# Kernel optimization log

Hardware: AMD Instinct MI355X
Metric: run time of the kernel (lower is better)

The kernel has to match this reference:

```python
import jax, jax.numpy as jnp
import numpy as np

SIGMA_MAX = 25.0

def marginal_prob_std(t):
    # VE-SDE std: sqrt((sigma_max^(2t) - 1) / (2 ln sigma_max))
    log_s = jnp.log(SIGMA_MAX)
    return jnp.sqrt((jnp.exp(2.0 * t * log_s) - 1.0) / (2.0 * log_s))

def setup_inputs() -> dict:
    key = jax.random.key(0)
    k1, k2, k3 = jax.random.split(key, 3)
    B, N, d = 16384, 16384, 1
    x = jax.random.normal(k1, (B, d), dtype=jnp.float32)
    t = jax.random.uniform(k2, (B,), dtype=jnp.float32, minval=1e-3, maxval=1.0)
    train_data = jax.random.normal(k3, (N, d), dtype=jnp.float32)
    return {"x": x, "t": t, "train_data": train_data}

def reference(x, t, train_data):
    # x: [B,1], t: [B], train_data: [N,1]
    sigma = marginal_prob_std(t)                       # [B]
    sigma2 = sigma * sigma                             # [B]
    # pairwise squared distance (d=1): [N, B]
    diff = train_data - x[:, 0][None, :]               # [N,1]-[1,B] -> broadcast fails; do explicit
    diff = train_data[:, 0][:, None] - x[:, 0][None, :]  # [N, B]
    pdf = jnp.exp(-0.5 * (diff * diff) / sigma2[None, :])  # [N, B]
    num = jnp.sum(pdf * train_data, axis=0)            # [N,B]*[N,1] -> [B]
    den = jnp.sum(pdf, axis=0)                         # [B]
    den_safe = jnp.where(den == 0.0, 1.0, den)
    evals = jnp.where(den == 0.0, 0.0, num / den_safe) # nan -> 0 as in torch code
    evals = evals[:, None]                             # [B,1]
    return (evals - x) / sigma2[:, None]
```

## Files before the change

### kernel.cpp

```cpp
#include <hip/hip_runtime.h>
#include <math.h>


typedef float v2f __attribute__((ext_vector_type(2)));
typedef float v8f __attribute__((ext_vector_type(8)));

#define BLK 256
#define CH  256
#define JPB (2 * BLK)

#if __has_builtin(__builtin_amdgcn_exp2f)
#define EXP2(x) __builtin_amdgcn_exp2f(x)
#else
#define EXP2(x) exp2f(x)
#endif

__device__ __forceinline__ float sigma2_of(float tj) {
  const float TWO_LOG_S = 6.4377516497364011f;
  return (__expf(TWO_LOG_S * tj) - 1.0f) / TWO_LOG_S;
}

template <bool ATOMIC>
__launch_bounds__(BLK)
__global__ void gmm_partial(const float* __restrict__ x,
                            const float* __restrict__ t,
                            const float* __restrict__ td,
                            float* __restrict__ ws,
                            int N, int B) {
  const int tid  = threadIdx.x;
  const int j0   = blockIdx.x * JPB + tid;
  const int j1   = j0 + BLK;
  const int s    = blockIdx.y;
  const int S    = gridDim.y;
  const int base = s * CH;
  const float* __restrict__ tp = td + base;
  const int lim = (N - base < CH) ? (N - base) : CH;

  const float HALF_LOG2E = 0.72134752044448170f;
  float r0 = 0.f, y0 = 0.f, r1 = 0.f, y1 = 0.f;
  if (j0 < B) { r0 = __fsqrt_rn(HALF_LOG2E / sigma2_of(t[j0])); y0 = x[j0] * r0; }
  if (j1 < B) { r1 = __fsqrt_rn(HALF_LOG2E / sigma2_of(t[j1])); y1 = x[j1] * r1; }

  const v2f rv0 = {r0, r0}, ny0 = {-y0, -y0};
  const v2f rv1 = {r1, r1}, ny1 = {-y1, -y1};

  v2f nA0 = {0,0}, nB0 = {0,0}, dA0 = {0,0}, dB0 = {0,0};
  v2f nA1 = {0,0}, nB1 = {0,0}, dA1 = {0,0}, dB1 = {0,0};

  auto body = [&](v2f g, const v2f& rv, const v2f& ny, v2f& nacc, v2f& dacc) {
    v2f d = __builtin_elementwise_fma(g, rv, ny);
    v2f q = d * d;
    v2f p;
    p.x = EXP2(-q.x);
    p.y = EXP2(-q.y);
    dacc += p;
    nacc = __builtin_elementwise_fma(p, g, nacc);
  };

  if (lim == CH) {
    #pragma unroll 2
    for (int i = 0; i < CH; i += 8) {
      v8f f = *(const v8f*)(tp + i);
      v2f g0 = {f[0], f[1]}, g1 = {f[2], f[3]};
      v2f g2 = {f[4], f[5]}, g3 = {f[6], f[7]};
      body(g0, rv0, ny0, nA0, dA0);
      body(g1, rv0, ny0, nB0, dB0);
      body(g2, rv0, ny0, nA0, dA0);
      body(g3, rv0, ny0, nB0, dB0);
      body(g0, rv1, ny1, nA1, dA1);
      body(g1, rv1, ny1, nB1, dB1);
      body(g2, rv1, ny1, nA1, dA1);
      body(g3, rv1, ny1, nB1, dB1);
    }
  } else {
    for (int i = 0; i < CH; i += 8) {
      v8f f;
      #pragma unroll
      for (int k = 0; k < 8; ++k) f[k] = (i + k < lim) ? tp[i + k] : 1e30f;
      v2f g0 = {f[0], f[1]}, g1 = {f[2], f[3]};
      v2f g2 = {f[4], f[5]}, g3 = {f[6], f[7]};
      body(g0, rv0, ny0, nA0, dA0);
      body(g1, rv0, ny0, nB0, dB0);
      body(g2, rv0, ny0, nA0, dA0);
      body(g3, rv0, ny0, nB0, dB0);
      body(g0, rv1, ny1, nA1, dA1);
      body(g1, rv1, ny1, nB1, dB1);
      body(g2, rv1, ny1, nA1, dA1);
      body(g3, rv1, ny1, nB1, dB1);
    }
  }

  v2f nv0 = nA0 + nB0, dv0 = dA0 + dB0;
  v2f nv1 = nA1 + nB1, dv1 = dA1 + dB1;
  float num0 = nv0.x + nv0.y, den0 = dv0.x + dv0.y;
  float num1 = nv1.x + nv1.y, den1 = dv1.x + dv1.y;

  if (ATOMIC) {
    if (j0 < B) { atomicAdd(&ws[j0], num0); atomicAdd(&ws[B + j0], den0); }
    if (j1 < B) { atomicAdd(&ws[j1], num1); atomicAdd(&ws[B + j1], den1); }
  } else {
    if (j0 < B) {
      ws[(size_t)s * B + j0]       = num0;
      ws[(size_t)(S + s) * B + j0] = den0;
    }
    if (j1 < B) {
      ws[(size_t)s * B + j1]       = num1;
      ws[(size_t)(S + s) * B + j1] = den1;
    }
  }
}

__global__ void gmm_final(const float* __restrict__ x,
                          const float* __restrict__ t,
                          const float* __restrict__ ws,
                          float* __restrict__ out, int B, int S) {
  int j = blockIdx.x * blockDim.x + threadIdx.x;
  if (j >= B) return;
  float num = 0.f, den = 0.f;
  for (int s = 0; s < S; ++s) {
    num += ws[(size_t)s * B + j];
    den += ws[(size_t)(S + s) * B + j];
  }
  float sigma2 = sigma2_of(t[j]);
  float evals = (den == 0.0f) ? 0.0f : (num / den);
  out[j] = (evals - x[j]) / sigma2;
}

__global__ void zero_kernel(float* __restrict__ p, int n) {
  int i = blockIdx.x * blockDim.x + threadIdx.x;
  if (i < n) p[i] = 0.0f;
}

extern "C" void kernel_launch(void* const* d_in, const int* in_sizes, int n_in,
                              void* d_out, int out_size, void* d_ws, size_t ws_size,
                              hipStream_t stream) {
  const float* x  = (const float*)d_in[0];
  const float* t  = (const float*)d_in[1];
  const float* td = (const float*)d_in[2];
  float* out = (float*)d_out;
  float* ws  = (float*)d_ws;

  const int B = in_sizes[0];
  const int N = in_sizes[2];

  const int S = (N + CH - 1) / CH;
  size_t need = (size_t)2 * S * B * sizeof(float);

  if (ws_size >= need) {
    dim3 grid((B + JPB - 1) / JPB, S);
    gmm_partial<false><<<grid, BLK, 0, stream>>>(x, t, td, ws, N, B);
    gmm_final<<<(B + BLK - 1) / BLK, BLK, 0, stream>>>(x, t, ws, out, B, S);
  } else {
    int nzero = 2 * B;
    zero_kernel<<<(nzero + 255) / 256, 256, 0, stream>>>(ws, nzero);
    dim3 grid((B + JPB - 1) / JPB, S);
    gmm_partial<true><<<grid, BLK, 0, stream>>>(x, t, td, ws, N, B);
    gmm_final<<<(B + BLK - 1) / BLK, BLK, 0, stream>>>(x, t, ws, out, B, 1);
  }
}
```

Measured before the change: 109.7 us.

## Process four outputs per thread with halved data chunks and software prefetch

Each thread now handles four B columns instead of two, so every loaded train_data value is reused across more outputs. The chunk size per block row is halved, giving twice as many partial slices, and the full-chunk loop prefetches the next 8-float vector before processing the current one. The aim is better amortization of loads and more independent exp work per thread. In exchange the partial workspace and the final reduction grow, and register pressure rises.

```diff
diff --git a/kernel.cpp b/kernel.cpp
--- a/kernel.cpp
+++ b/kernel.cpp
@@ -6,8 +6,9 @@
 typedef float v8f __attribute__((ext_vector_type(8)));
 
 #define BLK 256
-#define CH  256
-#define JPB (2 * BLK)
+#define CH  128
+#define JPT 4
+#define JPB (JPT * BLK)
 
 #if __has_builtin(__builtin_amdgcn_exp2f)
 #define EXP2(x) __builtin_amdgcn_exp2f(x)
@@ -28,84 +29,84 @@
                             float* __restrict__ ws,
                             int N, int B) {
   const int tid  = threadIdx.x;
-  const int j0   = blockIdx.x * JPB + tid;
-  const int j1   = j0 + BLK;
   const int s    = blockIdx.y;
   const int S    = gridDim.y;
   const int base = s * CH;
   const float* __restrict__ tp = td + base;
-  const int lim = (N - base < CH) ? (N - base) : CH;
 
   const float HALF_LOG2E = 0.72134752044448170f;
-  float r0 = 0.f, y0 = 0.f, r1 = 0.f, y1 = 0.f;
-  if (j0 < B) { r0 = __fsqrt_rn(HALF_LOG2E / sigma2_of(t[j0])); y0 = x[j0] * r0; }
-  if (j1 < B) { r1 = __fsqrt_rn(HALF_LOG2E / sigma2_of(t[j1])); y1 = x[j1] * r1; }
+  int   j[JPT];
+  v2f   rv[JPT], ny[JPT];
+  #pragma unroll
+  for (int k = 0; k < JPT; ++k) {
+    j[k] = blockIdx.x * JPB + k * BLK + tid;
+    float r = 0.f, y = 0.f;
+    if (j[k] < B) {
+      r = __fsqrt_rn(HALF_LOG2E / sigma2_of(t[j[k]]));
+      y = x[j[k]] * r;
+    }
+    rv[k].x = r;  rv[k].y = r;
+    ny[k].x = -y; ny[k].y = -y;
+  }
 
-  const v2f rv0 = {r0, r0}, ny0 = {-y0, -y0};
-  const v2f rv1 = {r1, r1}, ny1 = {-y1, -y1};
+  v2f nacc[JPT][2], dacc[JPT][2];
+  #pragma unroll
+  for (int k = 0; k < JPT; ++k)
+    #pragma unroll
+    for (int c = 0; c < 2; ++c) {
+      nacc[k][c].x = 0.f; nacc[k][c].y = 0.f;
+      dacc[k][c].x = 0.f; dacc[k][c].y = 0.f;
+    }
 
-  v2f nA0 = {0,0}, nB0 = {0,0}, dA0 = {0,0}, dB0 = {0,0};
-  v2f nA1 = {0,0}, nB1 = {0,0}, dA1 = {0,0}, dB1 = {0,0};
-
-  auto body = [&](v2f g, const v2f& rv, const v2f& ny, v2f& nacc, v2f& dacc) {
-    v2f d = __builtin_elementwise_fma(g, rv, ny);
-    v2f q = d * d;
-    v2f p;
-    p.x = EXP2(-q.x);
-    p.y = EXP2(-q.y);
-    dacc += p;
-    nacc = __builtin_elementwise_fma(p, g, nacc);
+  auto proc8 = [&](v8f f) {
+    v2f g[4] = {{f[0], f[1]}, {f[2], f[3]}, {f[4], f[5]}, {f[6], f[7]}};
+    #pragma unroll
+    for (int u = 0; u < 4; ++u) {
+      #pragma unroll
+      for (int k = 0; k < JPT; ++k) {
+        v2f d = __builtin_elementwise_fma(g[u], rv[k], ny[k]);
+        v2f q = d * d;
+        v2f p;
+        p.x = EXP2(-q.x);
+        p.y = EXP2(-q.y);
+        dacc[k][u & 1] += p;
+        nacc[k][u & 1] = __builtin_elementwise_fma(p, g[u], nacc[k][u & 1]);
+      }
+    }
   };
 
+  const int lim = (N - base < CH) ? (N - base) : CH;
   if (lim == CH) {
-    #pragma unroll 2
-    for (int i = 0; i < CH; i += 8) {
-      v8f f = *(const v8f*)(tp + i);
-      v2f g0 = {f[0], f[1]}, g1 = {f[2], f[3]};
-      v2f g2 = {f[4], f[5]}, g3 = {f[6], f[7]};
-      body(g0, rv0, ny0, nA0, dA0);
-      body(g1, rv0, ny0, nB0, dB0);
-      body(g2, rv0, ny0, nA0, dA0);
-      body(g3, rv0, ny0, nB0, dB0);
-      body(g0, rv1, ny1, nA1, dA1);
-      body(g1, rv1, ny1, nB1, dB1);
-      body(g2, rv1, ny1, nA1, dA1);
-      body(g3, rv1, ny1, nB1, dB1);
+    v8f f = *(const v8f*)(tp);
+    for (int i = 0; i < CH - 8; i += 8) {
+      v8f fn = *(const v8f*)(tp + i + 8);
+      proc8(f);
+      f = fn;
     }
+    proc8(f);
   } else {
-    for (int i = 0; i < CH; i += 8) {
+    for (int i = 0; i < lim; i += 8) {
       v8f f;
       #pragma unroll
-      for (int k = 0; k < 8; ++k) f[k] = (i + k < lim) ? tp[i + k] : 1e30f;
-      v2f g0 = {f[0], f[1]}, g1 = {f[2], f[3]};
-      v2f g2 = {f[4], f[5]}, g3 = {f[6], f[7]};
-      body(g0, rv0, ny0, nA0, dA0);
-      body(g1, rv0, ny0, nB0, dB0);
-      body(g2, rv0, ny0, nA0, dA0);
-      body(g3, rv0, ny0, nB0, dB0);
-      body(g0, rv1, ny1, nA1, dA1);
-      body(g1, rv1, ny1, nB1, dB1);
-      body(g2, rv1, ny1, nA1, dA1);
-      body(g3, rv1, ny1, nB1, dB1);
+      for (int e = 0; e < 8; ++e) f[e] = (i + e < lim) ? tp[i + e] : 1e30f;
+      proc8(f);
     }
   }
 
-  v2f nv0 = nA0 + nB0, dv0 = dA0 + dB0;
-  v2f nv1 = nA1 + nB1, dv1 = dA1 + dB1;
-  float num0 = nv0.x + nv0.y, den0 = dv0.x + dv0.y;
-  float num1 = nv1.x + nv1.y, den1 = dv1.x + dv1.y;
-
-  if (ATOMIC) {
-    if (j0 < B) { atomicAdd(&ws[j0], num0); atomicAdd(&ws[B + j0], den0); }
-    if (j1 < B) { atomicAdd(&ws[j1], num1); atomicAdd(&ws[B + j1], den1); }
-  } else {
-    if (j0 < B) {
-      ws[(size_t)s * B + j0]       = num0;
-      ws[(size_t)(S + s) * B + j0] = den0;
-    }
-    if (j1 < B) {
-      ws[(size_t)s * B + j1]       = num1;
-      ws[(size_t)(S + s) * B + j1] = den1;
+  #pragma unroll
+  for (int k = 0; k < JPT; ++k) {
+    v2f nv = nacc[k][0] + nacc[k][1];
+    v2f dv = dacc[k][0] + dacc[k][1];
+    float num = nv.x + nv.y;
+    float den = dv.x + dv.y;
+    if (j[k] < B) {
+      if (ATOMIC) {
+        atomicAdd(&ws[j[k]], num);
+        atomicAdd(&ws[B + j[k]], den);
+      } else {
+        ws[(size_t)s * B + j[k]]       = num;
+        ws[(size_t)(S + s) * B + j[k]] = den;
+      }
     }
   }
 }
```

After: 127.5 us. 1.16x slower.
